# Kernel optimization log

Hardware: AMD Instinct MI355X
Metric: run time of the kernel (lower is better)

The kernel has to match this reference:

```python
import jax, jax.numpy as jnp
import numpy as np

B, T, C_IN, C_OUT, H = 64, 512, 64, 64, 512


def setup_inputs() -> dict:
    key = jax.random.key(0)
    ks = jax.random.split(key, 24)
    s = 1.0 / np.sqrt(H)

    def p(k, shape):
        return (jax.random.uniform(k, shape, jnp.float32) * 2.0 - 1.0) * s

    inp = {
        "x": jax.random.normal(ks[0], (B, C_IN, T), jnp.float32),
        "frame_0": jax.random.normal(ks[1], (B, C_OUT, 1), jnp.float32),
    }
    i = 2
    for pre, in0 in (("enc", C_IN), ("dec", C_OUT)):
        for l, ins in enumerate((in0, H)):
            inp[f"{pre}_Wih{l}"] = p(ks[i], (3 * H, ins)); i += 1
            inp[f"{pre}_Whh{l}"] = p(ks[i], (3 * H, H)); i += 1
            inp[f"{pre}_bih{l}"] = p(ks[i], (3 * H,)); i += 1
            inp[f"{pre}_bhh{l}"] = p(ks[i], (3 * H,)); i += 1
    inp["fc_W"] = p(ks[i], (C_OUT, H)); i += 1
    inp["fc_b"] = p(ks[i], (C_OUT,))
    return inp


def _gru_cell(h, x, Wih, Whh, bih, bhh):
    # PyTorch GRU cell math: r,z,n gate ordering
    gi = x @ Wih.T + bih            # [B, 3H]
    gh = h @ Whh.T + bhh            # [B, 3H]
    ir, iz, inn = jnp.split(gi, 3, axis=-1)
    hr, hz, hn = jnp.split(gh, 3, axis=-1)
    r = jax.nn.sigmoid(ir + hr)
    z = jax.nn.sigmoid(iz + hz)
    n = jnp.tanh(inn + r * hn)
    return (1.0 - z) * n + z * h


def reference(x, frame_0,
              enc_Wih0, enc_Whh0, enc_bih0, enc_bhh0,
              enc_Wih1, enc_Whh1, enc_bih1, enc_bhh1,
              dec_Wih0, dec_Whh0, dec_bih0, dec_bhh0,
              dec_Wih1, dec_Whh1, dec_bih1, dec_bhh1,
              fc_W, fc_b):
    Bq = x.shape[0]
    num_steps = x.shape[-1]
    seq = jnp.transpose(x, (2, 0, 1))          # [T, B, C_in]
    f0 = frame_0[:, :, 0]                       # [B, C_out]

    enc_params = [(enc_Wih0, enc_Whh0, enc_bih0, enc_bhh0),
                  (enc_Wih1, enc_Whh1, enc_bih1, enc_bhh1)]
    dec_params = [(dec_Wih0, dec_Whh0, dec_bih0, dec_bhh0),
                  (dec_Wih1, dec_Whh1, dec_bih1, dec_bhh1)]

    # --- encoder: stacked GRU over T, zero initial hidden ---
    hiddens = []
    for (Wih, Whh, bih, bhh) in enc_params:
        h0 = jnp.zeros((Bq, Whh.shape[1]), seq.dtype)

        def step(h, xt, Wih=Wih, Whh=Whh, bih=bih, bhh=bhh):
            hn = _gru_cell(h, xt, Wih, Whh, bih, bhh)
            return hn, hn

        hT, seq = jax.lax.scan(step, h0, seq)   # seq becomes layer output [T,B,H]
        hiddens.append(hT)

    (W0, U0, b0, c0), (W1, U1, b1, c1) = dec_params

    def dec_step(carry, _):
        h0, h1, frame = carry
        h0n = _gru_cell(h0, frame, W0, U0, b0, c0)
        h1n = _gru_cell(h1, h0n, W1, U1, b1, c1)
        out = h1n @ fc_W.T + fc_b               # [B, C_out]
        return (h0n, h1n, out), out

    _, outs = jax.lax.scan(dec_step, (hiddens[0], hiddens[1], f0), None, length=num_steps)
    # outs: [T, B, C_out] -> (B, C_out, T)
    return jnp.transpose(outs, (1, 2, 0))
```

## Files before the change

### kernel.cpp

```cpp
#include <hip/hip_runtime.h>

#define H     512
#define BQ    64
#define TT    512
#define CIN   64
#define COUT  64
#define NWG   132
#define THREADS 256
#define RSLOTS 32

typedef unsigned int  uint;
typedef unsigned short ushort;
typedef unsigned long long u64;
typedef short bf16x8 __attribute__((ext_vector_type(8)));
typedef float f32x4  __attribute__((ext_vector_type(4)));

#define GH_BASE   0
#define GI_BASE   65536
#define GI0_BASE  131072
#define STG_BASE  139264
#define SMEM_SIZE 141312

#define WS_GF     0
#define WS_FA     8448
#define WS_FB     12544
#define WS_FF     16640
#define WS_BAR_SZ 20480
#define WS_BP     20480
#define WS_F0H    26624
#define WS_F0L    34816
#define WS_H0RH   65536
#define WS_H0RL   2162688
#define WS_H1RH   4259840
#define WS_H1RL   6356992
#define WS_M      8454144

#define SLOT(s)   (((s) & (RSLOTS-1)) * 32768)

struct Params {
  const float *x, *f0;
  const float *eWih0,*eWhh0,*ebih0,*ebhh0,*eWih1,*eWhh1,*ebih1,*ebhh1;
  const float *dWih0,*dWhh0,*dbih0,*dbhh0,*dWih1,*dWhh1,*dbih1,*dbhh1;
  const float *fcW,*fcb;
  float* out;
  char* ws;
};

__device__ __forceinline__ ushort f2bf(float v){
  uint b = __float_as_uint(v);
  return (ushort)((b + 0x7FFFu + ((b >> 16) & 1u)) >> 16);
}
__device__ __forceinline__ float bf2f(ushort u){ return __uint_as_float(((uint)u) << 16); }

__device__ __forceinline__ void waitS(const uint* __restrict__ f, uint thr, int tid){
  if (tid < 64){
    uint it = 0;
    while (__hip_atomic_load(&f[tid*16], __ATOMIC_RELAXED, __HIP_MEMORY_SCOPE_AGENT) < thr){
      __builtin_amdgcn_s_sleep(1);
      if ((++it & 1023u) == 0u) __builtin_amdgcn_fence(__ATOMIC_ACQUIRE, "agent");
    }
  }
  __syncthreads();
}
__device__ __forceinline__ void waitS4(const uint* __restrict__ f, uint thr, int tid){
  if (tid < 4){
    uint it = 0;
    while (__hip_atomic_load(&f[tid*16], __ATOMIC_RELAXED, __HIP_MEMORY_SCOPE_AGENT) < thr){
      __builtin_amdgcn_s_sleep(1);
      if ((++it & 1023u) == 0u) __builtin_amdgcn_fence(__ATOMIC_ACQUIRE, "agent");
    }
  }
  __syncthreads();
}
__device__ __forceinline__ void publish(uint* f, uint v){
  __hip_atomic_store(f, v, __ATOMIC_RELAXED, __HIP_MEMORY_SCOPE_AGENT);
}
__device__ __forceinline__ void invAll(){
  __builtin_amdgcn_fence(__ATOMIC_ACQUIRE, "agent");
}

__device__ __forceinline__ void gbar(uint* flags, uint r, int wg, int tid){
  __syncthreads();
  if (tid == 0){
    __builtin_amdgcn_fence(__ATOMIC_RELEASE, "agent");
    __hip_atomic_store(&flags[wg*16], r, __ATOMIC_RELAXED, __HIP_MEMORY_SCOPE_AGENT);
  }
  asm volatile("" ::: "memory");
  if (tid < NWG){
    uint it = 0;
    while (__hip_atomic_load(&flags[tid*16], __ATOMIC_RELAXED, __HIP_MEMORY_SCOPE_AGENT) < r){
      __builtin_amdgcn_s_sleep(1);
      if ((++it & 1023u) == 0u) __builtin_amdgcn_fence(__ATOMIC_ACQUIRE, "agent");
    }
  }
  __syncthreads();
  __builtin_amdgcn_fence(__ATOMIC_ACQUIRE, "agent");
}

template<int K>
__device__ void packW(char* lds, int base, const float* __restrict__ W, int colbase, int tid){
  for (int e = tid; e < 32*K; e += THREADS){
    int S = e / K, k = e - S*K;
    int gate = S & 3, hcl = S >> 2;
    float v = (gate < 3) ? W[(gate*H + colbase + hcl)*K + k] : 0.f;
    ushort hi = f2bf(v);
    ushort lo = f2bf(v - bf2f(hi));
    int tau = S >> 4, s = S & 15;
    int off = ((s*K + k)*2) ^ ((s & 7) << 4);
    char* tb = lds + base + tau*(16*K*4);
    *(ushort*)(tb + off) = hi;
    *(ushort*)(tb + 16*K*2 + off) = lo;
  }
}

__device__ void packFC(char* lds, const float* __restrict__ fcW, int colbase, int tid){
  for (int e = tid; e < 16*512; e += THREADS){
    int s = e >> 9, k = e & 511;
    float v = fcW[(colbase + s)*512 + k];
    ushort hi = f2bf(v);
    ushort lo = f2bf(v - bf2f(hi));
    int off = ((s*512 + k)*2) ^ ((s & 7) << 4);
    *(ushort*)(lds + off) = hi;
    *(ushort*)(lds + 16*512*2 + off) = lo;
  }
}

__device__ __forceinline__ void loadBias(const float* __restrict__ src, int colbase, int c, float* b){
#pragma unroll
  for (int tau = 0; tau < 2; ++tau){
    int gate = c & 3, hcl = 4*tau + (c >> 2);
    b[tau] = (gate < 3) ? src[gate*H + colbase + hcl] : 0.f;
  }
}

__device__ __forceinline__ void loadHold(const ushort* rh, const ushort* rl, int colb,
                                         int m, int lane, f32x4* hold){
  int c = lane & 15, g = lane >> 4;
#pragma unroll
  for (int tau = 0; tau < 2; ++tau){
    int col = colb + 4*tau + (c >> 2);
#pragma unroll
    for (int q = 0; q < 4; ++q){
      int row = m*16 + g*4 + q;
      int off = (col >> 3)*512 + row*8 + (col & 7);
      hold[tau][q] = bf2f(rh[off]) + bf2f(rl[off]);
    }
  }
}

template<int NTAU, int K, bool BLK>
__device__ __forceinline__ void gemm(const ushort* __restrict__ AH, const ushort* __restrict__ AL,
                                     const char* lds, int base, const float* bias,
                                     int m, int lane, f32x4* pre){
  const int c = lane & 15, g = lane >> 4;
  const int row = m*16 + c;
  constexpr int NK = K/32;
  bf16x8 ahv[NK], alv[NK];
#pragma unroll
  for (int kc = 0; kc < NK; ++kc){
    const int aoff = BLK ? ((kc*4 + g)*512 + row*8) : (row*K + kc*32 + g*8);
    ahv[kc] = *(const bf16x8*)(AH + aoff);
    alv[kc] = *(const bf16x8*)(AL + aoff);
  }
  f32x4 a1[NTAU], a2[NTAU];
#pragma unroll
  for (int tau = 0; tau < NTAU; ++tau){
    a1[tau] = f32x4{bias[tau], bias[tau], bias[tau], bias[tau]};
    a2[tau] = f32x4{0.f, 0.f, 0.f, 0.f};
  }
#pragma unroll
  for (int kc = 0; kc < NK; ++kc){
    const int off = ((c*K + kc*32 + g*8)*2) ^ ((c & 7) << 4);
#pragma unroll
    for (int tau = 0; tau < NTAU; ++tau){
      const char* tb = lds + base + tau*(16*K*4);
      bf16x8 wh = *(const bf16x8*)(tb + off);
      bf16x8 wl = *(const bf16x8*)(tb + 16*K*2 + off);
      a1[tau] = __builtin_amdgcn_mfma_f32_16x16x32_bf16(ahv[kc], wh, a1[tau], 0, 0, 0);
      a2[tau] = __builtin_amdgcn_mfma_f32_16x16x32_bf16(ahv[kc], wl, a2[tau], 0, 0, 0);
      a2[tau] = __builtin_amdgcn_mfma_f32_16x16x32_bf16(alv[kc], wh, a2[tau], 0, 0, 0);
    }
  }
#pragma unroll
  for (int tau = 0; tau < NTAU; ++tau) pre[tau] = a1[tau] + a2[tau];
}

__device__ __forceinline__ void gates_stage(const f32x4* pgi, const f32x4* pgh, f32x4* hold,
                                            ushort* __restrict__ stH, ushort* __restrict__ stL,
                                            int m, int lane){
  const int c = lane & 15, g = lane >> 4;
#pragma unroll
  for (int tau = 0; tau < 2; ++tau){
    f32x4 s, n, hn, rsh, zsh;
#pragma unroll
    for (int q = 0; q < 4; ++q) s[q] = 1.f / (1.f + expf(-(pgi[tau][q] + pgh[tau][q])));
#pragma unroll
    for (int q = 0; q < 4; ++q) rsh[q] = __shfl_xor(s[q], 2, 64);
#pragma unroll
    for (int q = 0; q < 4; ++q) zsh[q] = __shfl_xor(s[q], 3, 64);
#pragma unroll
    for (int q = 0; q < 4; ++q) n[q] = tanhf(pgi[tau][q] + rsh[q]*pgh[tau][q]);
#pragma unroll
    for (int q = 0; q < 4; ++q) hn[q] = (1.f - zsh[q])*n[q] + zsh[q]*hold[tau][q];
    hold[tau] = hn;
    if ((c & 3) == 2){
      const int cl = 4*tau + (c >> 2);
#pragma unroll
      for (int q = 0; q < 4; ++q){
        const int row = m*16 + g*4 + q;
        ushort hi = f2bf(hn[q]);
        ushort lo = f2bf(hn[q] - bf2f(hi));
        stH[row*8 + cl] = hi;
        stL[row*8 + cl] = lo;
      }
    }
  }
}

__device__ __forceinline__ void ring_flush(ushort* __restrict__ dH, ushort* __restrict__ dL,
                                           const ushort* __restrict__ stH,
                                           const ushort* __restrict__ stL, int tid){
  if (tid < 128){
    u64 v = *(const u64*)(stH + tid*4);
    __hip_atomic_store((u64*)dH + tid, v, __ATOMIC_RELAXED, __HIP_MEMORY_SCOPE_AGENT);
  } else if (tid < 256){
    int t2 = tid - 128;
    u64 v = *(const u64*)(stL + t2*4);
    __hip_atomic_store((u64*)dL + t2, v, __ATOMIC_RELAXED, __HIP_MEMORY_SCOPE_AGENT);
  }
}

__device__ __forceinline__ f32x4 bc4(float v){ return f32x4{v, v, v, v}; }

__global__ __launch_bounds__(THREADS, 1) void rnn_persist(Params p){
  extern __shared__ char smem[];
  char* ws = p.ws;
  uint* gflags = (uint*)(ws + WS_GF);
  uint* fA     = (uint*)(ws + WS_FA);
  uint* fB     = (uint*)(ws + WS_FB);
  uint* fF     = (uint*)(ws + WS_FF);
  float*  bp   = (float*)(ws + WS_BP);
  ushort* f0H  = (ushort*)(ws + WS_F0H);
  ushort* f0L  = (ushort*)(ws + WS_F0L);
  ushort* h0rH = (ushort*)(ws + WS_H0RH);
  ushort* h0rL = (ushort*)(ws + WS_H0RL);
  ushort* h1rH = (ushort*)(ws + WS_H1RH);
  ushort* h1rL = (ushort*)(ws + WS_H1RL);
  float*  Mw   = (float*)(ws + WS_M);
  ushort* xTH  = (ushort*)(void*)p.out;
  ushort* xTL  = xTH + TT*BQ*CIN;
  ushort* stH  = (ushort*)(smem + STG_BASE);
  ushort* stL  = stH + 512;

  const int wg = blockIdx.x, tid = threadIdx.x;
  const int wid = tid >> 6, lane = tid & 63;
  const int c = lane & 15;
  const int gtid = wg*THREADS + tid;
  const int gstride = NWG*THREADS;

  for (int e = gtid; e < TT*BQ*CIN; e += gstride){
    int t = e >> 12, b = (e >> 6) & 63, cc = e & 63;
    float v = p.x[(b*CIN + cc)*TT + t];
    ushort hi = f2bf(v);
    xTH[e] = hi; xTL[e] = f2bf(v - bf2f(hi));
  }
  for (int e = gtid; e < BQ*COUT; e += gstride){
    float v = p.f0[e];
    ushort hi = f2bf(v);
    f0H[e] = hi; f0L[e] = f2bf(v - bf2f(hi));
  }
  {
    const int total = 1536*512;
    const int per = (total + gstride - 1) / gstride;
    const int start = gtid * per;
    for (int i = 0; i < per; ++i){
      int e = start + i;
      if (e >= total) break;
      int rr = e >> 9, q = e & 511;
      float acc = 0.f;
      for (int k = 0; k < 64; ++k) acc += p.dWih0[rr*64 + k] * p.fcW[k*512 + q];
      Mw[e] = acc;
    }
  }
  for (int e = gtid; e < 1536; e += gstride){
    float acc = p.dbih0[e];
    for (int k = 0; k < 64; ++k) acc += p.dWih0[e*64 + k] * p.fcb[k];
    bp[e] = acc;
  }
  gbar(gflags, 1, wg, tid);

  const bool isA = (wg < 64), isB = (wg >= 64 && wg < 128);
  const int colb = isA ? wg*8 : (wg - 64)*8;
  const int kblk = colb >> 3;
  float bgi[2] = {0.f,0.f}, bgh[2] = {0.f,0.f}, bgi0[2] = {0.f,0.f}, bfc = 0.f;
  f32x4 hold[2]; hold[0] = bc4(0.f); hold[1] = bc4(0.f);

  if (isA){
    packW<64 >(smem, GI_BASE, p.eWih0, colb, tid);
    packW<512>(smem, GH_BASE, p.eWhh0, colb, tid);
    loadBias(p.ebih0, colb, c, bgi); loadBias(p.ebhh0, colb, c, bgh);
    __syncthreads();
    for (int t = 0; t < TT; ++t){
      if ((t & 15) == 0 && t > 0) invAll();
      f32x4 pgi[2], pgh[2];
      if (t > 0){
        waitS(fA, (uint)t, tid);
        gemm<2,512,true>(h0rH + SLOT(t-1), h0rL + SLOT(t-1), smem, GH_BASE, bgh, wid, lane, pgh);
      } else { pgh[0] = bc4(bgh[0]); pgh[1] = bc4(bgh[1]); }
      gemm<2,64,false>(xTH + t*4096, xTL + t*4096, smem, GI_BASE, bgi, wid, lane, pgi);
      if (t >= 32 && (t & 15) == 0) waitS(fB, (uint)(t-16), tid);
      gates_stage(pgi, pgh, hold, stH, stL, wid, lane);
      __syncthreads();
      ring_flush(h0rH + SLOT(t) + kblk*512, h0rL + SLOT(t) + kblk*512, stH, stL, tid);
      __syncthreads();
      if (tid == 0) publish(&fA[wg*16], (uint)(t+1));
    }
    __syncthreads();
    packW<512>(smem, GH_BASE, p.dWhh0, colb, tid);
    packW<512>(smem, GI_BASE, Mw,      colb, tid);
    packW<64 >(smem, GI0_BASE, p.dWih0, colb, tid);
    loadBias(bp,      colb, c, bgi);
    loadBias(p.dbhh0, colb, c, bgh);
    loadBias(p.dbih0, colb, c, bgi0);
    __syncthreads();
    waitS(fA, (uint)TT, tid);
    invAll();
    loadHold(h0rH + SLOT(511), h0rL + SLOT(511), colb, wid, lane, hold);
    for (int t = 0; t < TT; ++t){
      const int g = 512 + t;
      if ((t & 15) == 0 && t > 0) invAll();
      f32x4 pgi[2], pgh[2];
      waitS(fA, (uint)g, tid);
      gemm<2,512,true>(h0rH + SLOT(g-1), h0rL + SLOT(g-1), smem, GH_BASE, bgh, wid, lane, pgh);
      if (t == 0){
        waitS(fB, 481u, tid);
        gemm<2,64,false>(f0H, f0L, smem, GI0_BASE, bgi0, wid, lane, pgi);
      } else {
        waitS(fB, (uint)g, tid);
        gemm<2,512,true>(h1rH + SLOT(g-1), h1rL + SLOT(g-1), smem, GI_BASE, bgi, wid, lane, pgi);
      }
      gates_stage(pgi, pgh, hold, stH, stL, wid, lane);
      __syncthreads();
      ring_flush(h0rH + SLOT(g) + kblk*512, h0rL + SLOT(g) + kblk*512, stH, stL, tid);
      __syncthreads();
      if (tid == 0) publish(&fA[wg*16], (uint)(g+1));
    }
  } else if (isB){
    packW<512>(smem, GI_BASE, p.eWih1, colb, tid);
    packW<512>(smem, GH_BASE, p.eWhh1, colb, tid);
    loadBias(p.ebih1, colb, c, bgi); loadBias(p.ebhh1, colb, c, bgh);
    __syncthreads();
    for (int t = 0; t < TT; ++t){
      if ((t & 15) == 0 && t > 0) invAll();
      f32x4 pgi[2], pgh[2];
      if (t > 0){
        waitS(fB, (uint)t, tid);
        gemm<2,512,true>(h1rH + SLOT(t-1), h1rL + SLOT(t-1), smem, GH_BASE, bgh, wid, lane, pgh);
      } else { pgh[0] = bc4(bgh[0]); pgh[1] = bc4(bgh[1]); }
      waitS(fA, (uint)(t+1), tid);
      gemm<2,512,true>(h0rH + SLOT(t), h0rL + SLOT(t), smem, GI_BASE, bgi, wid, lane, pgi);
      gates_stage(pgi, pgh, hold, stH, stL, wid, lane);
      __syncthreads();
      ring_flush(h1rH + SLOT(t) + kblk*512, h1rL + SLOT(t) + kblk*512, stH, stL, tid);
      __syncthreads();
      if (tid == 0) publish(&fB[wg*16 - 64*16], (uint)(t+1));
    }
    __syncthreads();
    packW<512>(smem, GI_BASE, p.dWih1, colb, tid);
    packW<512>(smem, GH_BASE, p.dWhh1, colb, tid);
    loadBias(p.dbih1, colb, c, bgi); loadBias(p.dbhh1, colb, c, bgh);
    __syncthreads();
    waitS(fB, (uint)TT, tid);
    invAll();
    loadHold(h1rH + SLOT(511), h1rL + SLOT(511), colb, wid, lane, hold);
    for (int t = 0; t < TT; ++t){
      const int g = 512 + t;
      if ((t & 15) == 0 && t > 0) invAll();
      f32x4 pgi[2], pgh[2];
      waitS(fB, (uint)g, tid);
      gemm<2,512,true>(h1rH + SLOT(g-1), h1rL + SLOT(g-1), smem, GH_BASE, bgh, wid, lane, pgh);
      if (t >= 32 && (t & 15) == 0) waitS4(fF, (uint)(t-16), tid);
      waitS(fA, (uint)(g+1), tid);
      gemm<2,512,true>(h0rH + SLOT(g), h0rL + SLOT(g), smem, GI_BASE, bgi, wid, lane, pgi);
      gates_stage(pgi, pgh, hold, stH, stL, wid, lane);
      __syncthreads();
      ring_flush(h1rH + SLOT(g) + kblk*512, h1rL + SLOT(g) + kblk*512, stH, stL, tid);
      __syncthreads();
      if (tid == 0) publish(&fB[wg*16 - 64*16], (uint)(g+1));
    }
  } else {
    const int fccol = (wg - 128)*16;
    packFC(smem, p.fcW, fccol, tid);
    bfc = p.fcb[fccol + c];
    __syncthreads();
    for (int t = 0; t < TT; ++t){
      const int g = 512 + t;
      if ((t & 15) == 0) invAll();
      waitS(fB, (uint)(g+1), tid);
      f32x4 pre[1];
      gemm<1,512,true>(h1rH + SLOT(g), h1rL + SLOT(g), smem, 0, &bfc, wid, lane, pre);
      const int outcol = fccol + c, gq = lane >> 4;
#pragma unroll
      for (int q = 0; q < 4; ++q){
        const int row = wid*16 + gq*4 + q;
        p.out[(row*COUT + outcol)*TT + t] = pre[0][q];
      }
      __syncthreads();
      if (tid == 0) publish(&fF[(wg-128)*16], (uint)(t+1));
    }
  }
}

extern "C" void kernel_launch(void* const* d_in, const int* in_sizes, int n_in,
                              void* d_out, int out_size, void* d_ws, size_t ws_size,
                              hipStream_t stream){
  Params p;
  p.x     = (const float*)d_in[0];  p.f0    = (const float*)d_in[1];
  p.eWih0 = (const float*)d_in[2];  p.eWhh0 = (const float*)d_in[3];
  p.ebih0 = (const float*)d_in[4];  p.ebhh0 = (const float*)d_in[5];
  p.eWih1 = (const float*)d_in[6];  p.eWhh1 = (const float*)d_in[7];
  p.ebih1 = (const float*)d_in[8];  p.ebhh1 = (const float*)d_in[9];
  p.dWih0 = (const float*)d_in[10]; p.dWhh0 = (const float*)d_in[11];
  p.dbih0 = (const float*)d_in[12]; p.dbhh0 = (const float*)d_in[13];
  p.dWih1 = (const float*)d_in[14]; p.dWhh1 = (const float*)d_in[15];
  p.dbih1 = (const float*)d_in[16]; p.dbhh1 = (const float*)d_in[17];
  p.fcW   = (const float*)d_in[18]; p.fcb   = (const float*)d_in[19];
  p.out = (float*)d_out;
  p.ws  = (char*)d_ws;

  hipFuncSetAttribute((const void*)rnn_persist, hipFuncAttributeMaxDynamicSharedMemorySize, SMEM_SIZE);
  hipMemsetAsync(d_ws, 0, WS_BAR_SZ, stream);
  hipLaunchKernelGGL(rnn_persist, dim3(NWG), dim3(THREADS), SMEM_SIZE, stream, p);
}
```

Baseline: 10.28 ms.

## Replace block-wide flag waits with per-wave chunked waits inside GEMM loads

Block-level spin-waits followed by __syncthreads are replaced with wave-local polling using __all, so each wavefront proceeds on its own once its flags are ready. The 512-wide GEMM now waits per 16-producer chunk and loads that slice of the hidden state as soon as it is published, overlapping A-operand loads with still-arriving producers. This removes block barriers on the critical recurrent path but makes every wave poll global flags separately, which adds memory traffic and relies on the memory-ordering assumptions holding without a block sync.

```diff
diff --git a/kernel.cpp b/kernel.cpp
--- a/kernel.cpp
+++ b/kernel.cpp
@@ -52,25 +52,38 @@
 }
 __device__ __forceinline__ float bf2f(ushort u){ return __uint_as_float(((uint)u) << 16); }
 
-__device__ __forceinline__ void waitS(const uint* __restrict__ f, uint thr, int tid){
-  if (tid < 64){
-    uint it = 0;
-    while (__hip_atomic_load(&f[tid*16], __ATOMIC_RELAXED, __HIP_MEMORY_SCOPE_AGENT) < thr){
-      __builtin_amdgcn_s_sleep(1);
-      if ((++it & 1023u) == 0u) __builtin_amdgcn_fence(__ATOMIC_ACQUIRE, "agent");
-    }
-  }
-  __syncthreads();
-}
-__device__ __forceinline__ void waitS4(const uint* __restrict__ f, uint thr, int tid){
-  if (tid < 4){
-    uint it = 0;
-    while (__hip_atomic_load(&f[tid*16], __ATOMIC_RELAXED, __HIP_MEMORY_SCOPE_AGENT) < thr){
-      __builtin_amdgcn_s_sleep(1);
-      if ((++it & 1023u) == 0u) __builtin_amdgcn_fence(__ATOMIC_ACQUIRE, "agent");
-    }
-  }
-  __syncthreads();
+__device__ __forceinline__ void waitW16(const uint* __restrict__ f, int ch, uint thr, int lane){
+  uint it = 0;
+  for (;;){
+    int ok = 1;
+    if (lane < 16)
+      ok = (int)(__hip_atomic_load(&f[(ch*16 + lane)*16], __ATOMIC_RELAXED, __HIP_MEMORY_SCOPE_AGENT) >= thr);
+    if (__all(ok)) break;
+    __builtin_amdgcn_s_sleep(1);
+    if ((++it & 1023u) == 0u) __builtin_amdgcn_fence(__ATOMIC_ACQUIRE, "agent");
+  }
+  asm volatile("" ::: "memory");
+}
+__device__ __forceinline__ void waitWall(const uint* __restrict__ f, uint thr, int lane){
+  uint it = 0;
+  for (;;){
+    if (__all((int)(__hip_atomic_load(&f[lane*16], __ATOMIC_RELAXED, __HIP_MEMORY_SCOPE_AGENT) >= thr))) break;
+    __builtin_amdgcn_s_sleep(1);
+    if ((++it & 1023u) == 0u) __builtin_amdgcn_fence(__ATOMIC_ACQUIRE, "agent");
+  }
+  asm volatile("" ::: "memory");
+}
+__device__ __forceinline__ void waitW4(const uint* __restrict__ f, uint thr, int lane){
+  uint it = 0;
+  for (;;){
+    int ok = 1;
+    if (lane < 4)
+      ok = (int)(__hip_atomic_load(&f[lane*16], __ATOMIC_RELAXED, __HIP_MEMORY_SCOPE_AGENT) >= thr);
+    if (__all(ok)) break;
+    __builtin_amdgcn_s_sleep(1);
+    if ((++it & 1023u) == 0u) __builtin_amdgcn_fence(__ATOMIC_ACQUIRE, "agent");
+  }
+  asm volatile("" ::: "memory");
 }
 __device__ __forceinline__ void publish(uint* f, uint v){
   __hip_atomic_store(f, v, __ATOMIC_RELAXED, __HIP_MEMORY_SCOPE_AGENT);
@@ -148,19 +161,24 @@
   }
 }
 
-template<int NTAU, int K, bool BLK>
-__device__ __forceinline__ void gemm(const ushort* __restrict__ AH, const ushort* __restrict__ AL,
-                                     const char* lds, int base, const float* bias,
-                                     int m, int lane, f32x4* pre){
+template<int NTAU>
+__device__ __forceinline__ void gemm512p(const ushort* __restrict__ AH, const ushort* __restrict__ AL,
+                                         const char* lds, int base, const float* bias,
+                                         const uint* __restrict__ fl, uint thr,
+                                         int m, int lane, f32x4* pre){
   const int c = lane & 15, g = lane >> 4;
   const int row = m*16 + c;
-  constexpr int NK = K/32;
-  bf16x8 ahv[NK], alv[NK];
-#pragma unroll
-  for (int kc = 0; kc < NK; ++kc){
-    const int aoff = BLK ? ((kc*4 + g)*512 + row*8) : (row*K + kc*32 + g*8);
-    ahv[kc] = *(const bf16x8*)(AH + aoff);
-    alv[kc] = *(const bf16x8*)(AL + aoff);
+  bf16x8 ahv[16], alv[16];
+#pragma unroll
+  for (int ch = 0; ch < 4; ++ch){
+    waitW16(fl, ch, thr, lane);
+#pragma unroll
+    for (int j = 0; j < 4; ++j){
+      const int kc = ch*4 + j;
+      const int aoff = (kc*4 + g)*512 + row*8;
+      ahv[kc] = *(const bf16x8*)(AH + aoff);
+      alv[kc] = *(const bf16x8*)(AL + aoff);
+    }
   }
   f32x4 a1[NTAU], a2[NTAU];
 #pragma unroll
@@ -169,13 +187,49 @@
     a2[tau] = f32x4{0.f, 0.f, 0.f, 0.f};
   }
 #pragma unroll
-  for (int kc = 0; kc < NK; ++kc){
-    const int off = ((c*K + kc*32 + g*8)*2) ^ ((c & 7) << 4);
+  for (int kc = 0; kc < 16; ++kc){
+    const int off = ((c*512 + kc*32 + g*8)*2) ^ ((c & 7) << 4);
 #pragma unroll
     for (int tau = 0; tau < NTAU; ++tau){
-      const char* tb = lds + base + tau*(16*K*4);
+      const char* tb = lds + base + tau*(16*512*4);
       bf16x8 wh = *(const bf16x8*)(tb + off);
-      bf16x8 wl = *(const bf16x8*)(tb + 16*K*2 + off);
+      bf16x8 wl = *(const bf16x8*)(tb + 16*512*2 + off);
+      a1[tau] = __builtin_amdgcn_mfma_f32_16x16x32_bf16(ahv[kc], wh, a1[tau], 0, 0, 0);
+      a2[tau] = __builtin_amdgcn_mfma_f32_16x16x32_bf16(ahv[kc], wl, a2[tau], 0, 0, 0);
+      a2[tau] = __builtin_amdgcn_mfma_f32_16x16x32_bf16(alv[kc], wh, a2[tau], 0, 0, 0);
+    }
+  }
+#pragma unroll
+  for (int tau = 0; tau < NTAU; ++tau) pre[tau] = a1[tau] + a2[tau];
+}
+
+template<int NTAU>
+__device__ __forceinline__ void gemm64(const ushort* __restrict__ AH, const ushort* __restrict__ AL,
+                                       const char* lds, int base, const float* bias,
+                                       int m, int lane, f32x4* pre){
+  const int c = lane & 15, g = lane >> 4;
+  const int row = m*16 + c;
+  bf16x8 ahv[2], alv[2];
+#pragma unroll
+  for (int kc = 0; kc < 2; ++kc){
+    const int aoff = row*64 + kc*32 + g*8;
+    ahv[kc] = *(const bf16x8*)(AH + aoff);
+    alv[kc] = *(const bf16x8*)(AL + aoff);
+  }
+  f32x4 a1[NTAU], a2[NTAU];
+#pragma unroll
+  for (int tau = 0; tau < NTAU; ++tau){
+    a1[tau] = f32x4{bias[tau], bias[tau], bias[tau], bias[tau]};
+    a2[tau] = f32x4{0.f, 0.f, 0.f, 0.f};
+  }
+#pragma unroll
+  for (int kc = 0; kc < 2; ++kc){
+    const int off = ((c*64 + kc*32 + g*8)*2) ^ ((c & 7) << 4);
+#pragma unroll
+    for (int tau = 0; tau < NTAU; ++tau){
+      const char* tb = lds + base + tau*(16*64*4);
+      bf16x8 wh = *(const bf16x8*)(tb + off);
+      bf16x8 wl = *(const bf16x8*)(tb + 16*64*2 + off);
       a1[tau] = __builtin_amdgcn_mfma_f32_16x16x32_bf16(ahv[kc], wh, a1[tau], 0, 0, 0);
       a2[tau] = __builtin_amdgcn_mfma_f32_16x16x32_bf16(ahv[kc], wl, a2[tau], 0, 0, 0);
       a2[tau] = __builtin_amdgcn_mfma_f32_16x16x32_bf16(alv[kc], wh, a2[tau], 0, 0, 0);
@@ -303,12 +357,11 @@
     for (int t = 0; t < TT; ++t){
       if ((t & 15) == 0 && t > 0) invAll();
       f32x4 pgi[2], pgh[2];
-      if (t > 0){
-        waitS(fA, (uint)t, tid);
-        gemm<2,512,true>(h0rH + SLOT(t-1), h0rL + SLOT(t-1), smem, GH_BASE, bgh, wid, lane, pgh);
-      } else { pgh[0] = bc4(bgh[0]); pgh[1] = bc4(bgh[1]); }
-      gemm<2,64,false>(xTH + t*4096, xTL + t*4096, smem, GI_BASE, bgi, wid, lane, pgi);
-      if (t >= 32 && (t & 15) == 0) waitS(fB, (uint)(t-16), tid);
+      if (t > 0)
+        gemm512p<2>(h0rH + SLOT(t-1), h0rL + SLOT(t-1), smem, GH_BASE, bgh, fA, (uint)t, wid, lane, pgh);
+      else { pgh[0] = bc4(bgh[0]); pgh[1] = bc4(bgh[1]); }
+      gemm64<2>(xTH + t*4096, xTL + t*4096, smem, GI_BASE, bgi, wid, lane, pgi);
+      if (t >= 32 && (t & 15) == 0) waitWall(fB, (uint)(t-16), lane);
       gates_stage(pgi, pgh, hold, stH, stL, wid, lane);
       __syncthreads();
       ring_flush(h0rH + SLOT(t) + kblk*512, h0rL + SLOT(t) + kblk*512, stH, stL, tid);
@@ -323,21 +376,19 @@
     loadBias(p.dbhh0, colb, c, bgh);
     loadBias(p.dbih0, colb, c, bgi0);
     __syncthreads();
-    waitS(fA, (uint)TT, tid);
+    waitWall(fA, (uint)TT, lane);
     invAll();
     loadHold(h0rH + SLOT(511), h0rL + SLOT(511), colb, wid, lane, hold);
     for (int t = 0; t < TT; ++t){
       const int g = 512 + t;
       if ((t & 15) == 0 && t > 0) invAll();
       f32x4 pgi[2], pgh[2];
-      waitS(fA, (uint)g, tid);
-      gemm<2,512,true>(h0rH + SLOT(g-1), h0rL + SLOT(g-1), smem, GH_BASE, bgh, wid, lane, pgh);
+      gemm512p<2>(h0rH + SLOT(g-1), h0rL + SLOT(g-1), smem, GH_BASE, bgh, fA, (uint)g, wid, lane, pgh);
       if (t == 0){
-        waitS(fB, 481u, tid);
-        gemm<2,64,false>(f0H, f0L, smem, GI0_BASE, bgi0, wid, lane, pgi);
+        waitWall(fB, 481u, lane);
+        gemm64<2>(f0H, f0L, smem, GI0_BASE, bgi0, wid, lane, pgi);
       } else {
-        waitS(fB, (uint)g, tid);
-        gemm<2,512,true>(h1rH + SLOT(g-1), h1rL + SLOT(g-1), smem, GI_BASE, bgi, wid, lane, pgi);
+        gemm512p<2>(h1rH + SLOT(g-1), h1rL + SLOT(g-1), smem, GI_BASE, bgi, fB, (uint)g, wid, lane, pgi);
       }
       gates_stage(pgi, pgh, hold, stH, stL, wid, lane);
       __syncthreads();
@@ -353,40 +404,36 @@
     for (int t = 0; t < TT; ++t){
       if ((t & 15) == 0 && t > 0) invAll();
       f32x4 pgi[2], pgh[2];
-      if (t > 0){
-        waitS(fB, (uint)t, tid);
-        gemm<2,512,true>(h1rH + SLOT(t-1), h1rL + SLOT(t-1), smem, GH_BASE, bgh, wid, lane, pgh);
-      } else { pgh[0] = bc4(bgh[0]); pgh[1] = bc4(bgh[1]); }
-      waitS(fA, (uint)(t+1), tid);
-      gemm<2,512,true>(h0rH + SLOT(t), h0rL + SLOT(t), smem, GI_BASE, bgi, wid, lane, pgi);
+      if (t > 0)
+        gemm512p<2>(h1rH + SLOT(t-1), h1rL + SLOT(t-1), smem, GH_BASE, bgh, fB, (uint)t, wid, lane, pgh);
+      else { pgh[0] = bc4(bgh[0]); pgh[1] = bc4(bgh[1]); }
+      gemm512p<2>(h0rH + SLOT(t), h0rL + SLOT(t), smem, GI_BASE, bgi, fA, (uint)(t+1), wid, lane, pgi);
       gates_stage(pgi, pgh, hold, stH, stL, wid, lane);
       __syncthreads();
       ring_flush(h1rH + SLOT(t) + kblk*512, h1rL + SLOT(t) + kblk*512, stH, stL, tid);
       __syncthreads();
-      if (tid == 0) publish(&fB[wg*16 - 64*16], (uint)(t+1));
+      if (tid == 0) publish(&fB[(wg-64)*16], (uint)(t+1));
     }
     __syncthreads();
     packW<512>(smem, GI_BASE, p.dWih1, colb, tid);
     packW<512>(smem, GH_BASE, p.dWhh1, colb, tid);
     loadBias(p.dbih1, colb, c, bgi); loadBias(p.dbhh1, colb, c, bgh);
     __syncthreads();
-    waitS(fB, (uint)TT, tid);
+    waitWall(fB, (uint)TT, lane);
     invAll();
     loadHold(h1rH + SLOT(511), h1rL + SLOT(511), colb, wid, lane, hold);
     for (int t = 0; t < TT; ++t){
       const int g = 512 + t;
       if ((t & 15) == 0 && t > 0) invAll();
       f32x4 pgi[2], pgh[2];
-      waitS(fB, (uint)g, tid);
-      gemm<2,512,true>(h1rH + SLOT(g-1), h1rL + SLOT(g-1), smem, GH_BASE, bgh, wid, lane, pgh);
-      if (t >= 32 && (t & 15) == 0) waitS4(fF, (uint)(t-16), tid);
-      waitS(fA, (uint)(g+1), tid);
-      gemm<2,512,true>(h0rH + SLOT(g), h0rL + SLOT(g), smem, GI_BASE, bgi, wid, lane, pgi);
+      gemm512p<2>(h1rH + SLOT(g-1), h1rL + SLOT(g-1), smem, GH_BASE, bgh, fB, (uint)g, wid, lane, pgh);
+      if (t >= 32 && (t & 15) == 0) waitW4(fF, (uint)(t-16), lane);
+      gemm512p<2>(h0rH + SLOT(g), h0rL + SLOT(g), smem, GI_BASE, bgi, fA, (uint)(g+1), wid, lane, pgi);
       gates_stage(pgi, pgh, hold, stH, stL, wid, lane);
       __syncthreads();
       ring_flush(h1rH + SLOT(g) + kblk*512, h1rL + SLOT(g) + kblk*512, stH, stL, tid);
       __syncthreads();
-      if (tid == 0) publish(&fB[wg*16 - 64*16], (uint)(g+1));
+      if (tid == 0) publish(&fB[(wg-64)*16], (uint)(g+1));
     }
   } else {
     const int fccol = (wg - 128)*16;
@@ -396,9 +443,8 @@
     for (int t = 0; t < TT; ++t){
       const int g = 512 + t;
       if ((t & 15) == 0) invAll();
-      waitS(fB, (uint)(g+1), tid);
       f32x4 pre[1];
-      gemm<1,512,true>(h1rH + SLOT(g), h1rL + SLOT(g), smem, 0, &bfc, wid, lane, pre);
+      gemm512p<1>(h1rH + SLOT(g), h1rL + SLOT(g), smem, 0, &bfc, fB, (uint)(g+1), wid, lane, pre);
       const int outcol = fccol + c, gq = lane >> 4;
 #pragma unroll
       for (int q = 0; q < 4; ++q){
```

Result: slower. 10.76 ms (+4.6%).
